# Optimization experiments

Hardware: AMD Instinct MI355X
Metric: run time of the kernel (lower is better)

Reference implementation:

```python
import jax, jax.numpy as jnp
import numpy as np

N, H, W = 128, 400, 400          # instances, feature canvas
MS = 28                          # mask_size = pooler_resolution*2
CT, CS = 80, 53                  # thing / stuff classes
STRIDE = 4                       # common_stride
HG, WG = 1600, 1600              # image-resolution gt panoptic
IGNORE = 255
LOSS_W = 1.0


def setup_inputs() -> dict:
    key = jax.random.key(0)
    ks = jax.random.split(key, 8)
    mask_logits = jax.random.normal(ks[0], (N, CT, MS, MS), jnp.float32)
    stuff_logit = jax.random.normal(ks[1], (CS, H, W), jnp.float32)
    thing_logit = jax.random.normal(ks[2], (CT, H, W), jnp.float32)
    # valid boxes in image pixel coords (x0,y0,x2,y2), width/height >= 16 px
    x0 = jax.random.uniform(ks[3], (N,), minval=0.0, maxval=1200.0)
    y0 = jax.random.uniform(ks[4], (N,), minval=0.0, maxval=1200.0)
    wh = jax.random.uniform(ks[5], (N, 2), minval=16.0, maxval=400.0)
    x2 = jnp.minimum(x0 + wh[:, 0], WG - 1.0)
    y2 = jnp.minimum(y0 + wh[:, 1], HG - 1.0)
    bbox = jnp.stack([x0, y0, x2, y2], axis=1).astype(jnp.float32)
    cls_idx = jax.random.randint(ks[6], (N,), 0, CT, dtype=jnp.int32)
    gt_panoptic = jax.random.randint(ks[7], (HG, WG), 0, CS + N, dtype=jnp.int32)
    return {"mask_logits": mask_logits, "stuff_logit": stuff_logit,
            "thing_logit": thing_logit, "bbox": bbox, "cls_idx": cls_idx,
            "gt_panoptic": gt_panoptic}


def _axis_sample(lo, size, grid, src_size):
    """Bilinear sampling coords along one axis (align_corners=False).
    lo: [N] box start (feat px, int); size: [N] box extent; grid: [G].
    Returns (idx0, idx1, frac) each [N, G]."""
    dst = grid[None, :].astype(jnp.float32) - lo[:, None].astype(jnp.float32)
    src = (dst + 0.5) * (src_size / size[:, None].astype(jnp.float32)) - 0.5
    f = jnp.floor(src)
    t = src - f
    i0 = jnp.clip(f, 0, src_size - 1).astype(jnp.int32)
    i1 = jnp.clip(f + 1, 0, src_size - 1).astype(jnp.int32)
    return i0, i1, t


def reference(mask_logits, stuff_logit, thing_logit, bbox, cls_idx, gt_panoptic):
    # _separate_fetch_logits: gather per-instance class channel -> [N, MS, MS]
    ml = mask_logits[jnp.arange(N), cls_idx]

    # _unmap_mask_logit_single: boxes -> feat coords (.long() == floor, boxes >= 0)
    bl = jnp.floor(bbox / STRIDE).astype(jnp.int32)
    x0b, y0b, x2b, y2b = bl[:, 0], bl[:, 1], bl[:, 2], bl[:, 3]
    hh = y2b - y0b + 1
    ww = x2b - x0b + 1
    ys = jnp.arange(H, dtype=jnp.int32)
    xs = jnp.arange(W, dtype=jnp.int32)

    i0, i1, ty = _axis_sample(y0b, hh, ys, MS)   # [N, H]
    j0, j1, tx = _axis_sample(x0b, ww, xs, MS)   # [N, W]

    # separable bilinear: rows [N, H, MS] then cols [N, H, W]
    r0 = jnp.take_along_axis(ml, jnp.broadcast_to(i0[:, :, None], (N, H, MS)), axis=1)
    r1 = jnp.take_along_axis(ml, jnp.broadcast_to(i1[:, :, None], (N, H, MS)), axis=1)
    rows = r0 * (1.0 - ty)[:, :, None] + r1 * ty[:, :, None]
    c0 = jnp.take_along_axis(rows, jnp.broadcast_to(j0[:, None, :], (N, H, W)), axis=2)
    c1 = jnp.take_along_axis(rows, jnp.broadcast_to(j1[:, None, :], (N, H, W)), axis=2)
    val = c0 * (1.0 - tx)[:, None, :] + c1 * tx[:, None, :]

    vy = (ys[None, :] >= jnp.maximum(y0b, 0)[:, None]) & (ys[None, :] <= jnp.minimum(y2b, H - 1)[:, None])
    vx = (xs[None, :] >= jnp.maximum(x0b, 0)[:, None]) & (xs[None, :] <= jnp.minimum(x2b, W - 1)[:, None])
    thing_mask_logit = jnp.where(vy[:, :, None] & vx[:, None, :], val, 0.0)

    # _crop_thing_logit_single: int()/round() based crop window
    bf = bbox / STRIDE
    cx1 = bf[:, 0].astype(jnp.int32)
    cy1 = bf[:, 1].astype(jnp.int32)
    cx2 = (jnp.round(bf[:, 2]) + 1.0).astype(jnp.int32)
    cy2 = (jnp.round(bf[:, 3]) + 1.0).astype(jnp.int32)
    my = (ys[None, :] >= cy1[:, None]) & (ys[None, :] < cy2[:, None])
    mx = (xs[None, :] >= cx1[:, None]) & (xs[None, :] < cx2[:, None])
    thing_sem_logit = jnp.where(my[:, :, None] & mx[:, None, :], thing_logit[cls_idx], 0.0)

    pan_logit = jnp.concatenate(
        [stuff_logit[None], (thing_mask_logit + thing_sem_logit)[None]], axis=1)

    # gt nearest-downsample to feat_size, then CE with ignore_index
    iy = jnp.floor(jnp.arange(H) * (HG / H)).astype(jnp.int32)
    ix = jnp.floor(jnp.arange(W) * (WG / W)).astype(jnp.int32)
    gt_ds = gt_panoptic[iy[:, None], ix[None, :]][None]          # [1, H, W]
    logp = jax.nn.log_softmax(pan_logit, axis=1)
    tgt = jnp.clip(gt_ds, 0, CS + N - 1)
    nll = -jnp.take_along_axis(logp, tgt[:, None], axis=1)[:, 0]  # [1, H, W]
    valid = gt_ds != IGNORE
    pan_loss = LOSS_W * jnp.sum(jnp.where(valid, nll, 0.0)) / jnp.maximum(
        jnp.sum(valid).astype(jnp.float32), 1.0)
    return pan_logit, pan_loss
```

## Files before the change

kernel.cpp:

```cpp
#include <hip/hip_runtime.h>
#include <math.h>

#define N_   128
#define H_   400
#define W_   400
#define MS_  28
#define CT_  80
#define CS_  53
#define HW_  (H_*W_)
#define NCH_ (CS_ + N_)
#define WG_  1600
#define IGN_ 255
#define G_   8
#define CPG_ 23
#define PPT_ 4
#define BT_  256
#define PPB_ (BT_*PPT_)
#define GX_  ((HW_ + PPB_ - 1)/PPB_)

struct NParam {
  int vy_lo, vy_hi, vx_lo, vx_hi;
  int cy1, cy2, cx1, cx2;
  float sy, sx;
  int y0b, x0b;
  int mlbase, thbase;
  int pad0, pad1;
};

__device__ float        g_acc[2];
__device__ unsigned int g_done;
__device__ float        g_pm[G_*HW_];
__device__ float        g_ps[G_*HW_];

__device__ __forceinline__ void lse_update(float v, float& m, float& s) {
  float d = v - m;
  float e = __expf(-fabsf(d));
  s = (d > 0.0f) ? fmaf(s, e, 1.0f) : (s + e);
  m = fmaxf(m, v);
}

__global__ __launch_bounds__(256) void main_kernel(
    const float* __restrict__ mask_logits,
    const float* __restrict__ stuff_logit,
    const float* __restrict__ thing_logit,
    const float* __restrict__ bbox,
    const int*   __restrict__ cls_idx,
    float* __restrict__ out)
{
  __shared__ NParam spar[N_];
  int tid = threadIdx.x;
  if (blockIdx.x == 0 && blockIdx.y == 0 && tid == 0) {
    g_acc[0] = 0.0f; g_acc[1] = 0.0f; g_done = 0u;
  }
  if (tid < N_) {
    int n = tid;
    float b0 = bbox[4*n+0]*0.25f, b1 = bbox[4*n+1]*0.25f,
          b2 = bbox[4*n+2]*0.25f, b3 = bbox[4*n+3]*0.25f;
    int x0b = (int)floorf(b0), y0b = (int)floorf(b1);
    int x2b = (int)floorf(b2), y2b = (int)floorf(b3);
    int hh = y2b - y0b + 1, ww = x2b - x0b + 1;
    NParam p;
    p.vy_lo = max(y0b, 0); p.vy_hi = min(y2b, H_-1);
    p.vx_lo = max(x0b, 0); p.vx_hi = min(x2b, W_-1);
    p.cy1 = (int)b1; p.cx1 = (int)b0;
    p.cy2 = (int)(rintf(b3) + 1.0f);
    p.cx2 = (int)(rintf(b2) + 1.0f);
    p.sy = 28.0f / (float)hh; p.sx = 28.0f / (float)ww;
    p.y0b = y0b; p.x0b = x0b;
    int cls = cls_idx[n];
    p.mlbase = (n*CT_ + cls)*(MS_*MS_);
    p.thbase = cls*HW_;
    p.pad0 = 0; p.pad1 = 0;
    spar[n] = p;
  }
  __syncthreads();

  int pix0 = (blockIdx.x*BT_ + tid)*PPT_;
  if (pix0 >= HW_) return;
  int y  = pix0 / W_;
  int xb = pix0 - y*W_;

  int grp = blockIdx.y;
  int c0 = grp*CPG_;
  int c1 = min(NCH_, c0 + CPG_);

  float mv[PPT_], sv[PPT_];
  #pragma unroll
  for (int k = 0; k < PPT_; ++k) { mv[k] = -INFINITY; sv[k] = 0.0f; }

  int c = c0;
  for (; c < min(c1, CS_); ++c) {
    float4 v = *(const float4*)(stuff_logit + c*HW_ + pix0);
    *(float4*)(out + c*HW_ + pix0) = v;
    lse_update(v.x, mv[0], sv[0]);
    lse_update(v.y, mv[1], sv[1]);
    lse_update(v.z, mv[2], sv[2]);
    lse_update(v.w, mv[3], sv[3]);
  }
  for (; c < c1; ++c) {
    int n = c - CS_;
    NParam p = spar[n];
    float vv[PPT_] = {0.0f, 0.0f, 0.0f, 0.0f};
    if (y >= p.cy1 && y < p.cy2 && xb < p.cx2 && xb+PPT_-1 >= p.cx1) {
      float4 t = *(const float4*)(thing_logit + p.thbase + pix0);
      float tk[4] = {t.x, t.y, t.z, t.w};
      #pragma unroll
      for (int k = 0; k < PPT_; ++k) {
        int x = xb + k;
        if (x >= p.cx1 && x < p.cx2) vv[k] = tk[k];
      }
    }
    if (y >= p.vy_lo && y <= p.vy_hi && xb <= p.vx_hi && xb+PPT_-1 >= p.vx_lo) {
      float srcy = ((float)(y - p.y0b) + 0.5f)*p.sy - 0.5f;
      float fy = floorf(srcy); float ty = srcy - fy;
      int i0 = (int)fminf(fmaxf(fy,        0.0f), (float)(MS_-1));
      int i1 = (int)fminf(fmaxf(fy + 1.0f, 0.0f), (float)(MS_-1));
      const float* r0p = mask_logits + p.mlbase + i0*MS_;
      const float* r1p = mask_logits + p.mlbase + i1*MS_;
      #pragma unroll
      for (int k = 0; k < PPT_; ++k) {
        int x = xb + k;
        if (x >= p.vx_lo && x <= p.vx_hi) {
          float srcx = ((float)(x - p.x0b) + 0.5f)*p.sx - 0.5f;
          float fx = floorf(srcx); float tx = srcx - fx;
          int j0 = (int)fminf(fmaxf(fx,        0.0f), (float)(MS_-1));
          int j1 = (int)fminf(fmaxf(fx + 1.0f, 0.0f), (float)(MS_-1));
          float r0 = r0p[j0]*(1.0f - tx) + r0p[j1]*tx;
          float r1 = r1p[j0]*(1.0f - tx) + r1p[j1]*tx;
          vv[k] += r0*(1.0f - ty) + r1*ty;
        }
      }
    }
    *(float4*)(out + c*HW_ + pix0) = make_float4(vv[0], vv[1], vv[2], vv[3]);
    lse_update(vv[0], mv[0], sv[0]);
    lse_update(vv[1], mv[1], sv[1]);
    lse_update(vv[2], mv[2], sv[2]);
    lse_update(vv[3], mv[3], sv[3]);
  }

  *(float4*)(g_pm + grp*HW_ + pix0) = make_float4(mv[0], mv[1], mv[2], mv[3]);
  *(float4*)(g_ps + grp*HW_ + pix0) = make_float4(sv[0], sv[1], sv[2], sv[3]);
}

__global__ __launch_bounds__(256) void reduce_kernel(
    const int* __restrict__ gt,
    const float* __restrict__ out_ro,
    float* __restrict__ out)
{
  int tid = threadIdx.x;
  int pix0 = (blockIdx.x*BT_ + tid)*PPT_;
  float nll = 0.0f, cnt = 0.0f;
  if (pix0 < HW_) {
    float4 m4 = *(const float4*)(g_pm + pix0);
    float4 s4 = *(const float4*)(g_ps + pix0);
    float mv[PPT_] = {m4.x, m4.y, m4.z, m4.w};
    float sv[PPT_] = {s4.x, s4.y, s4.z, s4.w};
    #pragma unroll
    for (int g = 1; g < G_; ++g) {
      float4 mg4 = *(const float4*)(g_pm + g*HW_ + pix0);
      float4 sg4 = *(const float4*)(g_ps + g*HW_ + pix0);
      float mg[PPT_] = {mg4.x, mg4.y, mg4.z, mg4.w};
      float sg[PPT_] = {sg4.x, sg4.y, sg4.z, sg4.w};
      #pragma unroll
      for (int k = 0; k < PPT_; ++k) {
        float M = fmaxf(mv[k], mg[k]);
        sv[k] = sv[k]*__expf(mv[k] - M) + sg[k]*__expf(mg[k] - M);
        mv[k] = M;
      }
    }
    int y  = pix0 / W_;
    int xb = pix0 - y*W_;
    #pragma unroll
    for (int k = 0; k < PPT_; ++k) {
      int g = gt[y*(4*WG_) + (xb + k)*4];
      bool valid = (g != IGN_);
      int tc = min(max(g, 0), NCH_-1);
      float vt = out_ro[tc*HW_ + pix0 + k];
      nll += valid ? (mv[k] + __logf(sv[k]) - vt) : 0.0f;
      cnt += valid ? 1.0f : 0.0f;
    }
  }

  for (int off = 32; off >= 1; off >>= 1) {
    nll += __shfl_down(nll, off, 64);
    cnt += __shfl_down(cnt, off, 64);
  }
  __shared__ float red[8];
  int lane = tid & 63, wid = tid >> 6;
  if (lane == 0) { red[wid*2] = nll; red[wid*2+1] = cnt; }
  __syncthreads();
  if (tid == 0) {
    float ts  = red[0] + red[2] + red[4] + red[6];
    float tcn = red[1] + red[3] + red[5] + red[7];
    atomicAdd(&g_acc[0], ts);
    atomicAdd(&g_acc[1], tcn);
    __threadfence();
    unsigned int ticket = atomicAdd(&g_done, 1u);
    if (ticket == gridDim.x - 1) {
      __threadfence();
      float loss = g_acc[0] / fmaxf(g_acc[1], 1.0f);
      out[NCH_*HW_] = loss;
    }
  }
}

extern "C" void kernel_launch(void* const* d_in, const int* in_sizes, int n_in,
                              void* d_out, int out_size, void* d_ws, size_t ws_size,
                              hipStream_t stream) {
  const float* mask_logits = (const float*)d_in[0];
  const float* stuff_logit = (const float*)d_in[1];
  const float* thing_logit = (const float*)d_in[2];
  const float* bbox        = (const float*)d_in[3];
  const int*   cls_idx     = (const int*)d_in[4];
  const int*   gt          = (const int*)d_in[5];
  float* out = (float*)d_out;

  dim3 grid1(GX_, G_);
  main_kernel<<<grid1, BT_, 0, stream>>>(mask_logits, stuff_logit, thing_logit,
                                         bbox, cls_idx, out);
  reduce_kernel<<<GX_, BT_, 0, stream>>>(gt, out, out);
}
```

Measured before the change: 226.9 us.

## Fuse main and reduce kernels via per-column last-block ticket

Merges the two launches into one kernel. The last of the G channel-group blocks for each pixel column, chosen by an atomic ticket, combines the partial log-sum-exp values and computes the NLL. A global done counter then lets the final block write the loss and reset the accumulators for the next call. This removes one kernel launch and the gap between the two kernels. In exchange it adds atomics and fences, and it reads back the freshly written outputs from other blocks, which relies on the threadfence for correctness.

```diff
diff --git a/kernel.cpp b/kernel.cpp
--- a/kernel.cpp
+++ b/kernel.cpp
@@ -29,6 +29,7 @@
 
 __device__ float        g_acc[2];
 __device__ unsigned int g_done;
+__device__ unsigned int g_tick[GX_];
 __device__ float        g_pm[G_*HW_];
 __device__ float        g_ps[G_*HW_];
 
@@ -39,19 +40,20 @@
   m = fmaxf(m, v);
 }
 
-__global__ __launch_bounds__(256) void main_kernel(
+__global__ __launch_bounds__(256) void fused_kernel(
     const float* __restrict__ mask_logits,
     const float* __restrict__ stuff_logit,
     const float* __restrict__ thing_logit,
     const float* __restrict__ bbox,
     const int*   __restrict__ cls_idx,
-    float* __restrict__ out)
+    const int*   __restrict__ gt,
+    float* out)
 {
   __shared__ NParam spar[N_];
+  __shared__ unsigned int stick;
   int tid = threadIdx.x;
-  if (blockIdx.x == 0 && blockIdx.y == 0 && tid == 0) {
-    g_acc[0] = 0.0f; g_acc[1] = 0.0f; g_done = 0u;
-  }
+  int bx  = blockIdx.x, grp = blockIdx.y;
+
   if (tid < N_) {
     int n = tid;
     float b0 = bbox[4*n+0]*0.25f, b1 = bbox[4*n+1]*0.25f,
@@ -75,82 +77,85 @@
   }
   __syncthreads();
 
-  int pix0 = (blockIdx.x*BT_ + tid)*PPT_;
-  if (pix0 >= HW_) return;
-  int y  = pix0 / W_;
-  int xb = pix0 - y*W_;
-
-  int grp = blockIdx.y;
+  int pix0 = (bx*BT_ + tid)*PPT_;
+  bool act = (pix0 < HW_);
+  int y = 0, xb = 0;
+  if (act) { y = pix0 / W_; xb = pix0 - y*W_; }
+
   int c0 = grp*CPG_;
   int c1 = min(NCH_, c0 + CPG_);
 
-  float mv[PPT_], sv[PPT_];
-  #pragma unroll
-  for (int k = 0; k < PPT_; ++k) { mv[k] = -INFINITY; sv[k] = 0.0f; }
-
-  int c = c0;
-  for (; c < min(c1, CS_); ++c) {
-    float4 v = *(const float4*)(stuff_logit + c*HW_ + pix0);
-    *(float4*)(out + c*HW_ + pix0) = v;
-    lse_update(v.x, mv[0], sv[0]);
-    lse_update(v.y, mv[1], sv[1]);
-    lse_update(v.z, mv[2], sv[2]);
-    lse_update(v.w, mv[3], sv[3]);
-  }
-  for (; c < c1; ++c) {
-    int n = c - CS_;
-    NParam p = spar[n];
-    float vv[PPT_] = {0.0f, 0.0f, 0.0f, 0.0f};
-    if (y >= p.cy1 && y < p.cy2 && xb < p.cx2 && xb+PPT_-1 >= p.cx1) {
-      float4 t = *(const float4*)(thing_logit + p.thbase + pix0);
-      float tk[4] = {t.x, t.y, t.z, t.w};
-      #pragma unroll
-      for (int k = 0; k < PPT_; ++k) {
-        int x = xb + k;
-        if (x >= p.cx1 && x < p.cx2) vv[k] = tk[k];
-      }
-    }
-    if (y >= p.vy_lo && y <= p.vy_hi && xb <= p.vx_hi && xb+PPT_-1 >= p.vx_lo) {
-      float srcy = ((float)(y - p.y0b) + 0.5f)*p.sy - 0.5f;
-      float fy = floorf(srcy); float ty = srcy - fy;
-      int i0 = (int)fminf(fmaxf(fy,        0.0f), (float)(MS_-1));
-      int i1 = (int)fminf(fmaxf(fy + 1.0f, 0.0f), (float)(MS_-1));
-      const float* r0p = mask_logits + p.mlbase + i0*MS_;
-      const float* r1p = mask_logits + p.mlbase + i1*MS_;
-      #pragma unroll
-      for (int k = 0; k < PPT_; ++k) {
-        int x = xb + k;
-        if (x >= p.vx_lo && x <= p.vx_hi) {
-          float srcx = ((float)(x - p.x0b) + 0.5f)*p.sx - 0.5f;
-          float fx = floorf(srcx); float tx = srcx - fx;
-          int j0 = (int)fminf(fmaxf(fx,        0.0f), (float)(MS_-1));
-          int j1 = (int)fminf(fmaxf(fx + 1.0f, 0.0f), (float)(MS_-1));
-          float r0 = r0p[j0]*(1.0f - tx) + r0p[j1]*tx;
-          float r1 = r1p[j0]*(1.0f - tx) + r1p[j1]*tx;
-          vv[k] += r0*(1.0f - ty) + r1*ty;
+  if (act) {
+    float mv[PPT_], sv[PPT_];
+    #pragma unroll
+    for (int k = 0; k < PPT_; ++k) { mv[k] = -INFINITY; sv[k] = 0.0f; }
+
+    int c = c0;
+    int cs_end = min(c1, CS_);
+    for (; c < cs_end; ++c) {
+      float4 v = *(const float4*)(stuff_logit + c*HW_ + pix0);
+      *(float4*)(out + c*HW_ + pix0) = v;
+      lse_update(v.x, mv[0], sv[0]);
+      lse_update(v.y, mv[1], sv[1]);
+      lse_update(v.z, mv[2], sv[2]);
+      lse_update(v.w, mv[3], sv[3]);
+    }
+    for (; c < c1; ++c) {
+      int n = c - CS_;
+      NParam p = spar[n];
+      float vv[PPT_] = {0.0f, 0.0f, 0.0f, 0.0f};
+      if (y >= p.cy1 && y < p.cy2 && xb < p.cx2 && xb+PPT_-1 >= p.cx1) {
+        float4 t = *(const float4*)(thing_logit + p.thbase + pix0);
+        float tk[4] = {t.x, t.y, t.z, t.w};
+        #pragma unroll
+        for (int k = 0; k < PPT_; ++k) {
+          int x = xb + k;
+          if (x >= p.cx1 && x < p.cx2) vv[k] = tk[k];
         }
       }
-    }
-    *(float4*)(out + c*HW_ + pix0) = make_float4(vv[0], vv[1], vv[2], vv[3]);
-    lse_update(vv[0], mv[0], sv[0]);
-    lse_update(vv[1], mv[1], sv[1]);
-    lse_update(vv[2], mv[2], sv[2]);
-    lse_update(vv[3], mv[3], sv[3]);
-  }
-
-  *(float4*)(g_pm + grp*HW_ + pix0) = make_float4(mv[0], mv[1], mv[2], mv[3]);
-  *(float4*)(g_ps + grp*HW_ + pix0) = make_float4(sv[0], sv[1], sv[2], sv[3]);
-}
-
-__global__ __launch_bounds__(256) void reduce_kernel(
-    const int* __restrict__ gt,
-    const float* __restrict__ out_ro,
-    float* __restrict__ out)
-{
-  int tid = threadIdx.x;
-  int pix0 = (blockIdx.x*BT_ + tid)*PPT_;
+      if (y >= p.vy_lo && y <= p.vy_hi && xb <= p.vx_hi && xb+PPT_-1 >= p.vx_lo) {
+        float srcy = ((float)(y - p.y0b) + 0.5f)*p.sy - 0.5f;
+        float fy = floorf(srcy); float ty = srcy - fy;
+        int i0 = (int)fminf(fmaxf(fy,        0.0f), (float)(MS_-1));
+        int i1 = (int)fminf(fmaxf(fy + 1.0f, 0.0f), (float)(MS_-1));
+        const float* r0p = mask_logits + p.mlbase + i0*MS_;
+        const float* r1p = mask_logits + p.mlbase + i1*MS_;
+        #pragma unroll
+        for (int k = 0; k < PPT_; ++k) {
+          int x = xb + k;
+          if (x >= p.vx_lo && x <= p.vx_hi) {
+            float srcx = ((float)(x - p.x0b) + 0.5f)*p.sx - 0.5f;
+            float fx = floorf(srcx); float tx = srcx - fx;
+            int j0 = (int)fminf(fmaxf(fx,        0.0f), (float)(MS_-1));
+            int j1 = (int)fminf(fmaxf(fx + 1.0f, 0.0f), (float)(MS_-1));
+            float r0 = r0p[j0]*(1.0f - tx) + r0p[j1]*tx;
+            float r1 = r1p[j0]*(1.0f - tx) + r1p[j1]*tx;
+            vv[k] += r0*(1.0f - ty) + r1*ty;
+          }
+        }
+      }
+      *(float4*)(out + c*HW_ + pix0) = make_float4(vv[0], vv[1], vv[2], vv[3]);
+      lse_update(vv[0], mv[0], sv[0]);
+      lse_update(vv[1], mv[1], sv[1]);
+      lse_update(vv[2], mv[2], sv[2]);
+      lse_update(vv[3], mv[3], sv[3]);
+    }
+
+    *(float4*)(g_pm + grp*HW_ + pix0) = make_float4(mv[0], mv[1], mv[2], mv[3]);
+    *(float4*)(g_ps + grp*HW_ + pix0) = make_float4(sv[0], sv[1], sv[2], sv[3]);
+  }
+
+  __syncthreads();
+  if (tid == 0) {
+    __threadfence();
+    stick = atomicAdd(&g_tick[bx], 1u);
+  }
+  __syncthreads();
+  if (stick != G_ - 1) return;
+
+  __threadfence();
   float nll = 0.0f, cnt = 0.0f;
-  if (pix0 < HW_) {
+  if (act) {
     float4 m4 = *(const float4*)(g_pm + pix0);
     float4 s4 = *(const float4*)(g_ps + pix0);
     float mv[PPT_] = {m4.x, m4.y, m4.z, m4.w};
@@ -168,14 +173,12 @@
         mv[k] = M;
       }
     }
-    int y  = pix0 / W_;
-    int xb = pix0 - y*W_;
     #pragma unroll
     for (int k = 0; k < PPT_; ++k) {
       int g = gt[y*(4*WG_) + (xb + k)*4];
       bool valid = (g != IGN_);
       int tc = min(max(g, 0), NCH_-1);
-      float vt = out_ro[tc*HW_ + pix0 + k];
+      float vt = out[tc*HW_ + pix0 + k];
       nll += valid ? (mv[k] + __logf(sv[k]) - vt) : 0.0f;
       cnt += valid ? 1.0f : 0.0f;
     }
@@ -194,12 +197,14 @@
     float tcn = red[1] + red[3] + red[5] + red[7];
     atomicAdd(&g_acc[0], ts);
     atomicAdd(&g_acc[1], tcn);
+    g_tick[bx] = 0;
     __threadfence();
-    unsigned int ticket = atomicAdd(&g_done, 1u);
-    if (ticket == gridDim.x - 1) {
+    unsigned int d = atomicAdd(&g_done, 1u);
+    if (d == GX_ - 1) {
       __threadfence();
       float loss = g_acc[0] / fmaxf(g_acc[1], 1.0f);
       out[NCH_*HW_] = loss;
+      g_acc[0] = 0.0f; g_acc[1] = 0.0f; g_done = 0u;
     }
   }
 }
@@ -215,8 +220,7 @@
   const int*   gt          = (const int*)d_in[5];
   float* out = (float*)d_out;
 
-  dim3 grid1(GX_, G_);
-  main_kernel<<<grid1, BT_, 0, stream>>>(mask_logits, stuff_logit, thing_logit,
-                                         bbox, cls_idx, out);
-  reduce_kernel<<<GX_, BT_, 0, stream>>>(gt, out, out);
+  dim3 grid(GX_, G_);
+  fused_kernel<<<grid, BT_, 0, stream>>>(mask_logits, stuff_logit, thing_logit,
+                                         bbox, cls_idx, gt, out);
 }
```

Measured after the change: 331.0 us. 45.9% more time.
